# Performance work log

Hardware: AMD Instinct MI355X
Metric: run time of the kernel (lower is better)

Reference implementation:

```python
import jax, jax.numpy as jnp
import numpy as np

N, D, H, B, TOPK, M, NLAB = 200000, 512, 512, 256, 2, 100, 2000

def setup_inputs():
    rng = np.random.default_rng(0)
    features = rng.standard_normal((N, D)).astype(np.float32) * 0.05
    labels = rng.integers(0, NLAB, size=N).astype(np.int32)
    # fixed-shape cluster membership table (replaces dynamic features[labels==lab]
    # + randperm subsampling to max_cluster_num=100 in the torch loop)
    order = np.argsort(labels, kind='stable').astype(np.int32)
    counts = np.bincount(labels, minlength=NLAB)
    offs = np.concatenate([[0], np.cumsum(counts)]).astype(np.int64)
    cluster_members = np.zeros((NLAB, M), np.int32)
    cluster_mask = np.zeros((NLAB, M), np.bool_)
    for c in range(NLAB):
        k = int(min(counts[c], M))
        cluster_members[c, :k] = order[offs[c]:offs[c] + k]
        cluster_mask[c, :k] = True
    indexes = rng.integers(0, N, size=B).astype(np.int32)
    # neighbors guaranteed != indexes so neighbor labels are never the -1 placeholder
    neighbors = ((indexes[:, None] + 1 + rng.integers(0, N - 1, size=(B, TOPK))) % N).astype(np.int32)
    all_pred = rng.random((B, TOPK)).astype(np.float32)
    # GraphConv weight [2D,H] (cat(self, agg)), classifier Linear-PReLU-Linear(2)
    W1 = (rng.standard_normal((2 * D, H)) / np.sqrt(2 * D)).astype(np.float32)
    b1 = np.zeros(H, np.float32)
    W2 = (rng.standard_normal((H, H)) / np.sqrt(H)).astype(np.float32)
    b2 = np.zeros(H, np.float32)
    prelu_a = np.full(H, 0.25, np.float32)  # PReLU default init
    W3 = (rng.standard_normal((H, 2)) / np.sqrt(H)).astype(np.float32)
    b3 = np.zeros(2, np.float32)
    arrs = dict(features=features, labels=labels, indexes=indexes, neighbors=neighbors,
                all_pred=all_pred, cluster_members=cluster_members, cluster_mask=cluster_mask,
                W1=W1, b1=b1, W2=W2, b2=b2, prelu_a=prelu_a, W3=W3, b3=b3)
    return {k: jnp.asarray(v) for k, v in arrs.items()}

def _gcnl_loss(features, labels, indexes, neighbors, all_pred, cluster_members, cluster_mask,
               W1, b1, W2, b2, prelu_a, W3, b3):
    Bn = indexes.shape[0]
    sel = all_pred >= all_pred[:, :1]                    # neighbor kept if pred[:topk] >= pred[0]
    cand = labels[neighbors]                             # [B,2] candidate labels
    dup = (cand[:, 1] == cand[:, 0]) & sel[:, 0]         # torch.unique over the <=2 selected labels
    valid = jnp.stack([sel[:, 0], sel[:, 1] & ~dup], axis=1)  # [B,2]
    members = cluster_members[cand]                      # [B,2,M]
    # labels[indexes[i]] = -1 in the loop => sample never in its own cluster
    mmask = cluster_mask[cand] & (members != indexes[:, None, None])
    mfeats = features[members] * mmask[..., None].astype(features.dtype)  # [B,2,M,D] zero-padded
    x0 = features[indexes]                               # [B,D]
    x0k = jnp.broadcast_to(x0[:, None, None, :], (Bn, TOPK, 1, x0.shape[-1]))
    x = jnp.concatenate([x0k, mfeats], axis=2)           # [B,2,M+1,D] = cat(self, cluster)
    # adj = x @ x.T ; only row 0 feeds the loss (pred[0]), zero-padded rows contribute 0
    a0 = jnp.einsum('bkd,bkmd->bkm', x[:, :, 0], x)      # [B,2,M+1] adjacency row 0
    agg0 = jnp.einsum('bkm,bkmd->bkd', a0, x)            # MeanAggregator (A @ x) row 0
    cat0 = jnp.concatenate([x[:, :, 0], agg0], axis=-1)  # [B,2,2D]
    h0 = jax.nn.relu(jnp.einsum('bkd,df->bkf', cat0, W1) + b1)  # GraphConv row 0
    z = jnp.einsum('bkf,fg->bkg', h0, W2) + b2
    z = jnp.where(z >= 0, z, prelu_a * z)                # PReLU
    logits = jnp.einsum('bkg,gc->bkc', z, W3) + b3       # [B,2,2]
    gt = (cand == -1).astype(jnp.int32)                  # labels[idx] was -1 during the loop
    logp = jax.nn.log_softmax(logits, axis=-1)
    ce = -jnp.take_along_axis(logp, gt[..., None], axis=-1)[..., 0]  # [B,2]
    loss = jnp.sum(ce * valid.astype(ce.dtype)) / Bn
    return loss * 10.0

def reference(features, labels, indexes, neighbors, all_pred, cluster_members, cluster_mask,
              W1, b1, W2, b2, prelu_a, W3, b3):
    return _gcnl_loss(features, labels, indexes, neighbors, all_pred, cluster_members, cluster_mask,
                      W1, b1, W2, b2, prelu_a, W3, b3)
```

## Files before the change

kernel.cpp:

```cpp
#include <hip/hip_runtime.h>
#include <math.h>

#define N_PTS 200000
#define D 512
#define H 512
#define BATCH 256
#define TOPK 2
#define MCAP 100

typedef __attribute__((ext_vector_type(8))) short bf16x8;
typedef __attribute__((ext_vector_type(4))) float f32x4;

__device__ inline unsigned short f2bf(float f) {
    unsigned int u = __float_as_uint(f);
    u += 0x7FFFu + ((u >> 16) & 1u);
    return (unsigned short)(u >> 16);
}

__global__ __launch_bounds__(512, 4) void gather_prep_kernel(
    const float* __restrict__ features, const int* __restrict__ labels,
    const int* __restrict__ indexes, const int* __restrict__ neighbors,
    const float* __restrict__ all_pred, const int* __restrict__ cluster_members,
    const float* __restrict__ W1, const float* __restrict__ W2,
    unsigned short* __restrict__ W1t, unsigned short* __restrict__ W2t,
    unsigned short* __restrict__ cat0, float* __restrict__ validf, int* __restrict__ gts,
    float* __restrict__ out)
{
    int bid = blockIdx.x;
    int tid = threadIdx.x;

    if (bid >= 512) {
        __shared__ float tt[2][32][33];
        int t = (bid - 512) * 2 + (tid >> 8);
        int t256 = tid & 255;
        int tx = t256 & 31, ty = t256 >> 5;
        const float* src; unsigned short* dst; int R, C, bi;
        if (t < 512) { src = W1; dst = W1t; R = 1024; C = 512; bi = t; }
        else         { src = W2; dst = W2t; R = 512;  C = 512; bi = t - 512; }
        int nbc = C >> 5;
        int br = (bi / nbc) * 32, bc = (bi % nbc) * 32;
        int half = tid >> 8;
        #pragma unroll
        for (int i = 0; i < 32; i += 8)
            tt[half][ty + i][tx] = src[(size_t)(br + ty + i) * C + bc + tx];
        __syncthreads();
        #pragma unroll
        for (int i = 0; i < 32; i += 8)
            dst[(size_t)(bc + ty + i) * R + br + tx] = f2bf(tt[half][tx][ty + i]);
        return;
    }

    int bk = bid;
    int b = bk >> 1, k = bk & 1;
    int lane = tid & 63, w = tid >> 6;

    if (bk == 0 && tid == 0) out[0] = 0.0f;

    int idx  = indexes[b];
    int nb   = neighbors[b * TOPK + k];
    int c    = labels[nb];
    int lab0 = labels[0];

    const float4* frow0 = (const float4*)(features + (size_t)idx * D);
    float4 x0a = frow0[lane * 2];
    float4 x0b = frow0[lane * 2 + 1];

    const int NITER = 13;
    int   rowv[NITER];
    float wv[NITER];
    #pragma unroll
    for (int i = 0; i < NITER; ++i) {
        int m = w + i * 8;
        int row = idx; float wt = 0.0f;
        if (m == 0) {
            wt = 1.0f;
        } else if (m <= MCAP) {
            int mm = m - 1;
            int r2 = cluster_members[c * MCAP + mm];
            bool pad  = (r2 == 0) && !(c == lab0 && mm == 0);
            bool self = (r2 == idx);
            if (!pad && !self) { row = r2; wt = 1.0f; }
        }
        rowv[i] = row; wv[i] = wt;
    }

    float agg[8] = {0,0,0,0,0,0,0,0};

    const float4* fr0 = (const float4*)(features + (size_t)rowv[0] * D);
    float4 fa = fr0[lane * 2];
    float4 fb = fr0[lane * 2 + 1];
    #pragma unroll
    for (int i = 0; i < NITER; ++i) {
        float4 ca = fa, cb = fb;
        if (i + 1 < NITER) {
            const float4* nx = (const float4*)(features + (size_t)rowv[i + 1] * D);
            fa = nx[lane * 2];
            fb = nx[lane * 2 + 1];
        }
        float p = ca.x*x0a.x + ca.y*x0a.y + ca.z*x0a.z + ca.w*x0a.w
                + cb.x*x0b.x + cb.y*x0b.y + cb.z*x0b.z + cb.w*x0b.w;
        #pragma unroll
        for (int off = 32; off >= 1; off >>= 1) p += __shfl_xor(p, off);
        p *= wv[i];
        agg[0] += p * ca.x; agg[1] += p * ca.y; agg[2] += p * ca.z; agg[3] += p * ca.w;
        agg[4] += p * cb.x; agg[5] += p * cb.y; agg[6] += p * cb.z; agg[7] += p * cb.w;
    }

    __shared__ float aggl[8][D];
    #pragma unroll
    for (int j = 0; j < 8; ++j) aggl[w][lane * 8 + j] = agg[j];
    __syncthreads();

    unsigned short* crow = cat0 + (size_t)bk * (2 * D);
    if (w == 0) {
        union { unsigned short u[8]; uint4 q; } pk;
        pk.u[0] = f2bf(x0a.x); pk.u[1] = f2bf(x0a.y); pk.u[2] = f2bf(x0a.z); pk.u[3] = f2bf(x0a.w);
        pk.u[4] = f2bf(x0b.x); pk.u[5] = f2bf(x0b.y); pk.u[6] = f2bf(x0b.z); pk.u[7] = f2bf(x0b.w);
        ((uint4*)crow)[lane] = pk.q;
    }
    {
        float v = aggl[0][tid] + aggl[1][tid] + aggl[2][tid] + aggl[3][tid]
                + aggl[4][tid] + aggl[5][tid] + aggl[6][tid] + aggl[7][tid];
        crow[D + tid] = f2bf(v);
    }
    if (tid == 0) {
        float p0 = all_pred[b * TOPK];
        float pk = all_pred[b * TOPK + k];
        int cand0 = labels[neighbors[b * TOPK]];
        bool valid;
        if (k == 0) valid = true;
        else        valid = (pk >= p0) && (c != cand0);
        validf[bk] = valid ? 1.0f : 0.0f;
        gts[bk] = (c == -1) ? 1 : 0;
    }
}

__global__ __launch_bounds__(512) void gemm_bf16(
    const unsigned short* __restrict__ A, const unsigned short* __restrict__ Bt,
    const float* __restrict__ bias, int N, int K, int act,
    const float* __restrict__ pa, float* __restrict__ Cf, unsigned short* __restrict__ Cb)
{
    int tid = threadIdx.x;
    int lane = tid & 63, w = tid >> 6;
    int nbn = N >> 5;
    int row0 = (blockIdx.x / nbn) * 32, col0 = (blockIdx.x % nbn) * 32;

    int r = lane & 15;
    int kg = (lane >> 4) * 8;
    int kb = w * (K >> 3);

    const unsigned short* Ar0 = A  + (size_t)(row0 + r) * K + kb + kg;
    const unsigned short* Ar1 = Ar0 + (size_t)16 * K;
    const unsigned short* Br0 = Bt + (size_t)(col0 + r) * K + kb + kg;
    const unsigned short* Br1 = Br0 + (size_t)16 * K;

    f32x4 acc00 = {0,0,0,0}, acc01 = {0,0,0,0}, acc10 = {0,0,0,0}, acc11 = {0,0,0,0};

    int kchunk = K >> 3;
    for (int ks = 0; ks < kchunk; ks += 32) {
        bf16x8 a0 = *(const bf16x8*)(Ar0 + ks);
        bf16x8 a1 = *(const bf16x8*)(Ar1 + ks);
        bf16x8 b0 = *(const bf16x8*)(Br0 + ks);
        bf16x8 b1 = *(const bf16x8*)(Br1 + ks);
        acc00 = __builtin_amdgcn_mfma_f32_16x16x32_bf16(a0, b0, acc00, 0, 0, 0);
        acc01 = __builtin_amdgcn_mfma_f32_16x16x32_bf16(a0, b1, acc01, 0, 0, 0);
        acc10 = __builtin_amdgcn_mfma_f32_16x16x32_bf16(a1, b0, acc10, 0, 0, 0);
        acc11 = __builtin_amdgcn_mfma_f32_16x16x32_bf16(a1, b1, acc11, 0, 0, 0);
    }

    __shared__ float red[8][32][33];
    int rbase = (lane >> 4) * 4, cbase = lane & 15;
    #pragma unroll
    for (int j = 0; j < 4; ++j) {
        red[w][rbase + j][cbase]           = acc00[j];
        red[w][rbase + j][16 + cbase]      = acc01[j];
        red[w][16 + rbase + j][cbase]      = acc10[j];
        red[w][16 + rbase + j][16 + cbase] = acc11[j];
    }
    __syncthreads();

    for (int e = tid; e < 1024; e += 512) {
        int rr = e >> 5, cc = e & 31;
        float v = red[0][rr][cc] + red[1][rr][cc] + red[2][rr][cc] + red[3][rr][cc]
                + red[4][rr][cc] + red[5][rr][cc] + red[6][rr][cc] + red[7][rr][cc];
        int gc = col0 + cc;
        v += bias[gc];
        if (act == 0) {
            v = fmaxf(v, 0.f);
            Cb[(size_t)(row0 + rr) * N + gc] = f2bf(v);
        } else {
            v = (v >= 0.f) ? v : pa[gc] * v;
            Cf[(size_t)(row0 + rr) * N + gc] = v;
        }
    }
}

__global__ __launch_bounds__(256) void final_kernel(
    const float* __restrict__ z, const float* __restrict__ W3, const float* __restrict__ b3,
    const float* __restrict__ validf, const int* __restrict__ gts, float* __restrict__ out)
{
    int w = threadIdx.x >> 6, lane = threadIdx.x & 63;
    int bk = blockIdx.x * 4 + w;
    const float* zr = z + (size_t)bk * H;
    const float4* z4 = (const float4*)zr;
    float4 za = z4[lane * 2], zb = z4[lane * 2 + 1];
    const float4* w4 = (const float4*)W3;
    float l0 = 0, l1 = 0;
    float4 wp;
    wp = w4[lane * 4 + 0]; l0 += za.x * wp.x + za.y * wp.z; l1 += za.x * wp.y + za.y * wp.w;
    wp = w4[lane * 4 + 1]; l0 += za.z * wp.x + za.w * wp.z; l1 += za.z * wp.y + za.w * wp.w;
    wp = w4[lane * 4 + 2]; l0 += zb.x * wp.x + zb.y * wp.z; l1 += zb.x * wp.y + zb.y * wp.w;
    wp = w4[lane * 4 + 3]; l0 += zb.z * wp.x + zb.w * wp.z; l1 += zb.z * wp.y + zb.w * wp.w;
    #pragma unroll
    for (int off = 32; off >= 1; off >>= 1) {
        l0 += __shfl_xor(l0, off);
        l1 += __shfl_xor(l1, off);
    }
    if (lane == 0) {
        l0 += b3[0]; l1 += b3[1];
        int gt = gts[bk];
        float mx = fmaxf(l0, l1);
        float lse = mx + logf(expf(l0 - mx) + expf(l1 - mx));
        float sel = (gt == 0) ? l0 : l1;
        float ce = lse - sel;
        atomicAdd(out, ce * validf[bk] * (10.0f / (float)BATCH));
    }
}

extern "C" void kernel_launch(void* const* d_in, const int* in_sizes, int n_in,
                              void* d_out, int out_size, void* d_ws, size_t ws_size,
                              hipStream_t stream) {
    const float* features        = (const float*)d_in[0];
    const int*   labels          = (const int*)d_in[1];
    const int*   indexes         = (const int*)d_in[2];
    const int*   neighbors       = (const int*)d_in[3];
    const float* all_pred        = (const float*)d_in[4];
    const int*   cluster_members = (const int*)d_in[5];
    const float* W1 = (const float*)d_in[7];
    const float* b1 = (const float*)d_in[8];
    const float* W2 = (const float*)d_in[9];
    const float* b2 = (const float*)d_in[10];
    const float* pa = (const float*)d_in[11];
    const float* W3 = (const float*)d_in[12];
    const float* b3 = (const float*)d_in[13];
    float* out = (float*)d_out;

    char* ws = (char*)d_ws;
    float*          validf = (float*)(ws + 8192);
    int*            gts    = (int*)(ws + 10240);
    unsigned short* W1t    = (unsigned short*)(ws + 12288);
    unsigned short* W2t    = (unsigned short*)(ws + 1060864);
    unsigned short* cat0b  = (unsigned short*)(ws + 1585152);
    unsigned short* h0b    = (unsigned short*)(ws + 2633728);
    float*          zbuf   = (float*)(ws + 3158016);

    gather_prep_kernel<<<896, 512, 0, stream>>>(
        features, labels, indexes, neighbors, all_pred, cluster_members,
        W1, W2, W1t, W2t, cat0b, validf, gts, out);
    gemm_bf16<<<256, 512, 0, stream>>>(cat0b, W1t, b1, 512, 1024, 0, pa, nullptr, h0b);
    gemm_bf16<<<256, 512, 0, stream>>>(h0b,   W2t, b2, 512, 512,  1, pa, zbuf, nullptr);
    final_kernel<<<128, 256, 0, stream>>>(zbuf, W3, b3, validf, gts, out);
}
```

Baseline: 42.90 us.

## Fuse second GEMM with PReLU, classifier and loss into one kernel

Merges the second GEMM, the PReLU epilogue, the 512x2 classifier and the cross-entropy reduction into one kernel. Each block now computes 16 full rows across all 512 output columns, so the logits can be reduced in registers and shared memory without writing z to global memory. This removes one kernel launch and the z round trip, and cuts the number of atomics. It also specialises the first GEMM with compile-time shapes and full unrolling. The trade-off is that the fused kernel runs only 32 blocks, each looping over the full K=512 serially, which lowers parallelism.

New measurement: 49.71 us. +15.9%, slower.

```diff
diff --git a/kernel.cpp b/kernel.cpp
--- a/kernel.cpp
+++ b/kernel.cpp
@@ -135,15 +135,14 @@
     }
 }
 
-__global__ __launch_bounds__(512) void gemm_bf16(
+__global__ __launch_bounds__(512) void gemm1_kernel(
     const unsigned short* __restrict__ A, const unsigned short* __restrict__ Bt,
-    const float* __restrict__ bias, int N, int K, int act,
-    const float* __restrict__ pa, float* __restrict__ Cf, unsigned short* __restrict__ Cb)
+    const float* __restrict__ bias, unsigned short* __restrict__ Cb)
 {
+    const int N = 512, K = 1024;
     int tid = threadIdx.x;
     int lane = tid & 63, w = tid >> 6;
-    int nbn = N >> 5;
-    int row0 = (blockIdx.x / nbn) * 32, col0 = (blockIdx.x % nbn) * 32;
+    int row0 = (blockIdx.x >> 4) * 32, col0 = (blockIdx.x & 15) * 32;
 
     int r = lane & 15;
     int kg = (lane >> 4) * 8;
@@ -156,8 +155,8 @@
 
     f32x4 acc00 = {0,0,0,0}, acc01 = {0,0,0,0}, acc10 = {0,0,0,0}, acc11 = {0,0,0,0};
 
-    int kchunk = K >> 3;
-    for (int ks = 0; ks < kchunk; ks += 32) {
+    #pragma unroll
+    for (int ks = 0; ks < (K >> 3); ks += 32) {
         bf16x8 a0 = *(const bf16x8*)(Ar0 + ks);
         bf16x8 a1 = *(const bf16x8*)(Ar1 + ks);
         bf16x8 b0 = *(const bf16x8*)(Br0 + ks);
@@ -179,51 +178,102 @@
     }
     __syncthreads();
 
+    #pragma unroll
     for (int e = tid; e < 1024; e += 512) {
         int rr = e >> 5, cc = e & 31;
         float v = red[0][rr][cc] + red[1][rr][cc] + red[2][rr][cc] + red[3][rr][cc]
                 + red[4][rr][cc] + red[5][rr][cc] + red[6][rr][cc] + red[7][rr][cc];
         int gc = col0 + cc;
-        v += bias[gc];
-        if (act == 0) {
-            v = fmaxf(v, 0.f);
-            Cb[(size_t)(row0 + rr) * N + gc] = f2bf(v);
-        } else {
-            v = (v >= 0.f) ? v : pa[gc] * v;
-            Cf[(size_t)(row0 + rr) * N + gc] = v;
-        }
-    }
-}
-
-__global__ __launch_bounds__(256) void final_kernel(
-    const float* __restrict__ z, const float* __restrict__ W3, const float* __restrict__ b3,
-    const float* __restrict__ validf, const int* __restrict__ gts, float* __restrict__ out)
+        v = fmaxf(v + bias[gc], 0.0f);
+        Cb[(size_t)(row0 + rr) * N + gc] = f2bf(v);
+    }
+}
+
+__global__ __launch_bounds__(512) void gemm2_final_kernel(
+    const unsigned short* __restrict__ A, const unsigned short* __restrict__ Bt,
+    const float* __restrict__ b2, const float* __restrict__ pa,
+    const float* __restrict__ W3, const float* __restrict__ b3,
+    const float* __restrict__ validf, const int* __restrict__ gts,
+    float* __restrict__ out)
 {
-    int w = threadIdx.x >> 6, lane = threadIdx.x & 63;
-    int bk = blockIdx.x * 4 + w;
-    const float* zr = z + (size_t)bk * H;
-    const float4* z4 = (const float4*)zr;
-    float4 za = z4[lane * 2], zb = z4[lane * 2 + 1];
-    const float4* w4 = (const float4*)W3;
-    float l0 = 0, l1 = 0;
-    float4 wp;
-    wp = w4[lane * 4 + 0]; l0 += za.x * wp.x + za.y * wp.z; l1 += za.x * wp.y + za.y * wp.w;
-    wp = w4[lane * 4 + 1]; l0 += za.z * wp.x + za.w * wp.z; l1 += za.z * wp.y + za.w * wp.w;
-    wp = w4[lane * 4 + 2]; l0 += zb.x * wp.x + zb.y * wp.z; l1 += zb.x * wp.y + zb.y * wp.w;
-    wp = w4[lane * 4 + 3]; l0 += zb.z * wp.x + zb.w * wp.z; l1 += zb.z * wp.y + zb.w * wp.w;
-    #pragma unroll
-    for (int off = 32; off >= 1; off >>= 1) {
-        l0 += __shfl_xor(l0, off);
-        l1 += __shfl_xor(l1, off);
-    }
-    if (lane == 0) {
-        l0 += b3[0]; l1 += b3[1];
-        int gt = gts[bk];
+    const int K = 512;
+    int tid = threadIdx.x;
+    int lane = tid & 63, w = tid >> 6;
+    int row0 = blockIdx.x * 16;
+
+    int r = lane & 15;
+    int kg = (lane >> 4) * 8;
+
+    const unsigned short* Ar  = A + (size_t)(row0 + r) * K + kg;
+    const unsigned short* Br0 = Bt + (size_t)(w * 64 + 0  + r) * K + kg;
+    const unsigned short* Br1 = Bt + (size_t)(w * 64 + 16 + r) * K + kg;
+    const unsigned short* Br2 = Bt + (size_t)(w * 64 + 32 + r) * K + kg;
+    const unsigned short* Br3 = Bt + (size_t)(w * 64 + 48 + r) * K + kg;
+
+    f32x4 acc0 = {0,0,0,0}, acc1 = {0,0,0,0}, acc2 = {0,0,0,0}, acc3 = {0,0,0,0};
+
+    #pragma unroll
+    for (int ks = 0; ks < K; ks += 32) {
+        bf16x8 a  = *(const bf16x8*)(Ar + ks);
+        bf16x8 b0 = *(const bf16x8*)(Br0 + ks);
+        bf16x8 b1 = *(const bf16x8*)(Br1 + ks);
+        bf16x8 b2v = *(const bf16x8*)(Br2 + ks);
+        bf16x8 b3v = *(const bf16x8*)(Br3 + ks);
+        acc0 = __builtin_amdgcn_mfma_f32_16x16x32_bf16(a, b0,  acc0, 0, 0, 0);
+        acc1 = __builtin_amdgcn_mfma_f32_16x16x32_bf16(a, b1,  acc1, 0, 0, 0);
+        acc2 = __builtin_amdgcn_mfma_f32_16x16x32_bf16(a, b2v, acc2, 0, 0, 0);
+        acc3 = __builtin_amdgcn_mfma_f32_16x16x32_bf16(a, b3v, acc3, 0, 0, 0);
+    }
+
+    float q0[4] = {0,0,0,0}, q1[4] = {0,0,0,0};
+    {
+        f32x4 av[4] = {acc0, acc1, acc2, acc3};
+        #pragma unroll
+        for (int t = 0; t < 4; ++t) {
+            int gc = w * 64 + t * 16 + r;
+            float bb = b2[gc], aa = pa[gc];
+            float w30 = W3[gc * 2], w31 = W3[gc * 2 + 1];
+            #pragma unroll
+            for (int j = 0; j < 4; ++j) {
+                float v = av[t][j] + bb;
+                v = (v >= 0.0f) ? v : aa * v;
+                q0[j] += v * w30;
+                q1[j] += v * w31;
+            }
+        }
+    }
+    #pragma unroll
+    for (int off = 8; off >= 1; off >>= 1) {
+        #pragma unroll
+        for (int j = 0; j < 4; ++j) {
+            q0[j] += __shfl_xor(q0[j], off);
+            q1[j] += __shfl_xor(q1[j], off);
+        }
+    }
+
+    __shared__ float part[8][16][2];
+    if (r == 0) {
+        int rg = (lane >> 4) * 4;
+        #pragma unroll
+        for (int j = 0; j < 4; ++j) {
+            part[w][rg + j][0] = q0[j];
+            part[w][rg + j][1] = q1[j];
+        }
+    }
+    __syncthreads();
+
+    if (tid < 16) {
+        int bk = row0 + tid;
+        float l0 = b3[0], l1 = b3[1];
+        #pragma unroll
+        for (int q = 0; q < 8; ++q) { l0 += part[q][tid][0]; l1 += part[q][tid][1]; }
         float mx = fmaxf(l0, l1);
         float lse = mx + logf(expf(l0 - mx) + expf(l1 - mx));
-        float sel = (gt == 0) ? l0 : l1;
-        float ce = lse - sel;
-        atomicAdd(out, ce * validf[bk] * (10.0f / (float)BATCH));
+        float sel = gts[bk] ? l1 : l0;
+        float ce = (lse - sel) * validf[bk];
+        #pragma unroll
+        for (int off = 8; off >= 1; off >>= 1) ce += __shfl_xor(ce, off);
+        if (tid == 0) atomicAdd(out, ce * (10.0f / (float)BATCH));
     }
 }
 
@@ -252,12 +302,11 @@
     unsigned short* W2t    = (unsigned short*)(ws + 1060864);
     unsigned short* cat0b  = (unsigned short*)(ws + 1585152);
     unsigned short* h0b    = (unsigned short*)(ws + 2633728);
-    float*          zbuf   = (float*)(ws + 3158016);
 
     gather_prep_kernel<<<896, 512, 0, stream>>>(
         features, labels, indexes, neighbors, all_pred, cluster_members,
         W1, W2, W1t, W2t, cat0b, validf, gts, out);
-    gemm_bf16<<<256, 512, 0, stream>>>(cat0b, W1t, b1, 512, 1024, 0, pa, nullptr, h0b);
-    gemm_bf16<<<256, 512, 0, stream>>>(h0b,   W2t, b2, 512, 512,  1, pa, zbuf, nullptr);
-    final_kernel<<<128, 256, 0, stream>>>(zbuf, W3, b3, validf, gts, out);
-}
+    gemm1_kernel<<<256, 512, 0, stream>>>(cat0b, W1t, b1, h0b);
+    gemm2_final_kernel<<<32, 512, 0, stream>>>(h0b, W2t, b2, pa, W3, b3,
+                                               validf, gts, out);
+}
```
